# Kernel tuning notes

Hardware: AMD Instinct MI355X
Metric: run time of the kernel (lower is better)

## Reference

```python
import jax, jax.numpy as jnp
import numpy as np

N_NODES = 20000
N_EDGES = 200000
MUL = 16          # multiplicity of 0e and 1o in irreps_in/out
NUM_BASIS = 8
HIDDEN = 64
W_NUMEL = 4 * MUL * MUL  # 1024: four 'uvw' paths of 16x1x16 weights
INV_SQRT3 = 1.0 / np.sqrt(3.0)
PW0 = np.sqrt(1.0 / 32.0)  # path weight into 0e: sqrt(dim(0e)/(16+16))
PW1 = np.sqrt(3.0 / 32.0)  # path weight into 1o: sqrt(dim(1o)/(16+16))
SI_NORM = 1.0 / np.sqrt(MUL)  # o3.Linear fan-in normalization


def setup_inputs() -> dict:
    key = jax.random.key(0)
    ks = jax.random.split(key, 12)
    node_feat = jax.random.normal(ks[0], (N_NODES, 4 * MUL), dtype=jnp.float32)
    edge_attr = jax.random.uniform(ks[1], (N_EDGES, NUM_BASIS), dtype=jnp.float32)
    sh = jax.random.normal(ks[2], (N_EDGES, 4), dtype=jnp.float32)
    edge_index = jax.random.randint(ks[3], (2, N_EDGES), 0, N_NODES, dtype=jnp.int32)
    # radial MLP params (torch nn.Linear: y = x @ W.T + b; we store W already transposed)
    w1 = jax.random.normal(ks[4], (NUM_BASIS, HIDDEN), dtype=jnp.float32) * 0.3
    b1 = jax.random.normal(ks[5], (HIDDEN,), dtype=jnp.float32) * 0.1
    w2 = jax.random.normal(ks[6], (HIDDEN, W_NUMEL), dtype=jnp.float32) * 0.1
    b2 = jax.random.normal(ks[7], (W_NUMEL,), dtype=jnp.float32) * 0.1
    # o3.Linear self-interaction: one (mul_in, mul_out) block per irrep
    wsi0 = jax.random.normal(ks[8], (MUL, MUL), dtype=jnp.float32)
    wsi1 = jax.random.normal(ks[9], (MUL, MUL), dtype=jnp.float32)
    return {"node_feat": node_feat, "edge_attr": edge_attr, "sh": sh,
            "w1": w1, "b1": b1, "w2": w2, "b2": b2,
            "wsi0": wsi0, "wsi1": wsi1, "edge_index": edge_index}


def reference(node_feat, edge_attr, sh, w1, b1, w2, b2, wsi0, wsi1, edge_index):
    n_nodes = node_feat.shape[0]
    row, col = edge_index[0], edge_index[1]

    # per-edge tensor-product weights from radial basis
    h = jax.nn.silu(edge_attr @ w1 + b1)
    w = h @ w2 + b2                                   # [E, 1024]
    Wp = w.reshape(-1, 4, MUL, MUL)                    # 4 paths, each (u, w)

    # gathered source-node features, split into 0e scalars and 1o vectors
    xs = node_feat[col, :MUL]                          # [E, 16]
    xv = node_feat[col, MUL:].reshape(-1, MUL, 3)      # [E, 16, 3]
    y0 = sh[:, 0]                                      # [E]   0e part of sh
    y1 = sh[:, 1:4]                                    # [E,3] 1o part of sh

    # CG paths (e3nn FullyConnectedTensorProduct, component/element norm):
    # path0: 0e x 0e -> 0e (cg=1); path3: 1o x 1o -> 0e (cg=delta/sqrt3)
    dot = jnp.einsum('eum,em->eu', xv, y1)             # [E,16]
    out0 = PW0 * (jnp.einsum('euw,eu->ew', Wp[:, 0], xs * y0[:, None])
                  + INV_SQRT3 * jnp.einsum('euw,eu->ew', Wp[:, 3], dot))
    # path1: 0e x 1o -> 1o; path2: 1o x 0e -> 1o (cg=delta/sqrt3)
    outv = (PW1 * INV_SQRT3) * (
        jnp.einsum('euw,eu->ew', Wp[:, 1], xs)[:, :, None] * y1[:, None, :]
        + jnp.einsum('euw,eum->ewm', Wp[:, 2], xv) * y0[:, None, None])

    messages = jnp.concatenate([out0, outv.reshape(-1, 3 * MUL)], axis=-1)  # [E,64]
    agg = jax.ops.segment_sum(messages, row, num_segments=n_nodes)          # [N,64]

    # self-interaction: o3.Linear (block-diagonal per irrep, / sqrt(fan_in))
    si0 = (node_feat[:, :MUL] @ wsi0) * SI_NORM
    siv = jnp.einsum('num,uw->nwm', node_feat[:, MUL:].reshape(-1, MUL, 3), wsi1) * SI_NORM
    si = jnp.concatenate([si0, siv.reshape(-1, 3 * MUL)], axis=-1)
    return agg + si
```

## Files before the change

kernel.cpp:

```cpp
#include <hip/hip_runtime.h>
#include <hip/hip_bf16.h>

#define N_NODES_C 20000
#define N_EDGES_C 200000

#define PW0_C       0.17677669529663687f
#define PW1_C       0.30618621784789724f
#define INV_SQRT3_C 0.57735026918962576f
#define SI_NORM_C   0.25f

typedef __attribute__((ext_vector_type(8))) short short8;
typedef __attribute__((ext_vector_type(4))) float f32x4;

__device__ __forceinline__ unsigned short f2bf(float x) {
    union { float f; unsigned u; } v; v.f = x;
    unsigned r = v.u + 0x7fffu + ((v.u >> 16) & 1u);
    return (unsigned short)(r >> 16);
}

__global__ __launch_bounds__(256) void k_h(const float* __restrict__ ea,
                                           const float* __restrict__ w1,
                                           const float* __restrict__ b1,
                                           unsigned short* __restrict__ h) {
    int idx = blockIdx.x * 256 + threadIdx.x;
    int e = idx >> 6, c = idx & 63;
    const float* a = ea + e * 8;
    float acc = b1[c];
    #pragma unroll
    for (int k = 0; k < 8; ++k) acc = fmaf(a[k], w1[k * 64 + c], acc);
    float s = acc / (1.0f + __expf(-acc));
    h[idx] = f2bf(s);
}

__global__ __launch_bounds__(256) void k_w2(const float* __restrict__ w2,
                                            unsigned short* __restrict__ w2f) {
    int tid = blockIdx.x * 256 + threadIdx.x;
    int j  = tid & 7;
    int l  = (tid >> 3) & 63;
    int ks = (tid >> 9) & 1;
    int tp = tid >> 10;
    int u = tp >> 2, k = tp & 3;
    int krow = ks * 32 + (l >> 4) * 8 + j;
    int col  = k * 256 + u * 16 + (l & 15);
    w2f[tid] = f2bf(w2[krow * 1024 + col]);
}

__global__ __launch_bounds__(256) void k_si(const float* __restrict__ nf,
                                            const float* __restrict__ wsi0,
                                            const float* __restrict__ wsi1,
                                            float* __restrict__ out) {
    int idx = blockIdx.x * 256 + threadIdx.x;
    int n = idx >> 6, c = idx & 63;
    const float* x = nf + n * 64;
    float acc = 0.f;
    if (c < 16) {
        #pragma unroll
        for (int u = 0; u < 16; ++u) acc = fmaf(x[u], wsi0[u * 16 + c], acc);
    } else {
        int w = (c - 16) / 3, m = (c - 16) - w * 3;
        #pragma unroll
        for (int u = 0; u < 16; ++u) acc = fmaf(x[16 + u * 3 + m], wsi1[u * 16 + w], acc);
    }
    out[idx] = acc * SI_NORM_C;
}

__global__ __launch_bounds__(256) void k_main(const float* __restrict__ nf,
                                              const float* __restrict__ sh,
                                              const int* __restrict__ ei,
                                              const unsigned short* __restrict__ h,
                                              const unsigned short* __restrict__ w2f,
                                              const float* __restrict__ b2,
                                              float* __restrict__ out) {
    __shared__ unsigned short w2s[2][4096];
    __shared__ float S[6][16][64];
    __shared__ float sh_s[64][4];
    __shared__ float b2_s[4][16][16];
    __shared__ int   row_s[64];

    float (*nf_s)[64] = (float (*)[64])w2s;

    const int t    = threadIdx.x;
    const int e0   = blockIdx.x * 64;
    const int lane = t & 63;
    const int wid  = t >> 6;

    {
        float* b2flat = &b2_s[0][0][0];
        #pragma unroll
        for (int i = 0; i < 4; ++i) b2flat[t + i * 256] = b2[t + i * 256];
        int el = t >> 2, part = t & 3;
        int col = ei[N_EDGES_C + e0 + el];
        const f32x4* src = (const f32x4*)(nf + col * 64);
        #pragma unroll
        for (int q = 0; q < 4; ++q)
            *(f32x4*)&nf_s[el][part * 16 + q * 4] = src[part * 4 + q];
        if (part == 0) {
            *(f32x4*)&sh_s[el][0] = *(const f32x4*)(sh + (e0 + el) * 4);
            row_s[el] = ei[e0 + el];
        }
    }
    const unsigned short* hrow = h + (e0 + wid * 16 + (lane & 15)) * 64 + ((lane >> 4) * 8);
    short8 a0 = *(const short8*)(hrow);
    short8 a1 = *(const short8*)(hrow + 32);
    __syncthreads();

    int4 p0, p1;
    {
        const int4* wsrc = (const int4*)(w2f);
        p0 = wsrc[t]; p1 = wsrc[256 + t];
    }
    {
        int el = t >> 2, part = t & 3;
        float y0 = sh_s[el][0], y1x = sh_s[el][1], y1y = sh_s[el][2], y1z = sh_s[el][3];
        #pragma unroll
        for (int uu = 0; uu < 4; ++uu) {
            int u = part * 4 + uu;
            float xs = nf_s[el][u];
            float v0 = nf_s[el][16 + u * 3 + 0];
            float v1 = nf_s[el][16 + u * 3 + 1];
            float v2 = nf_s[el][16 + u * 3 + 2];
            float dot = v0 * y1x + v1 * y1y + v2 * y1z;
            S[0][u][el] = xs * y0;
            S[1][u][el] = xs;
            S[2][u][el] = v0;
            S[3][u][el] = v1;
            S[4][u][el] = v2;
            S[5][u][el] = INV_SQRT3_C * dot;
        }
    }
    __syncthreads();
    ((int4*)w2s[0])[t] = p0;
    ((int4*)w2s[0])[256 + t] = p1;
    __syncthreads();

    const int wcol = lane & 15;
    const int eS   = wid * 16 + ((lane >> 4) << 2);

    f32x4 acc0 = {0.f, 0.f, 0.f, 0.f};
    f32x4 tv1  = {0.f, 0.f, 0.f, 0.f};
    f32x4 t2a  = {0.f, 0.f, 0.f, 0.f};
    f32x4 t2b  = {0.f, 0.f, 0.f, 0.f};
    f32x4 t2c  = {0.f, 0.f, 0.f, 0.f};

    for (int u = 0; u < 16; ++u) {
        const int buf = u & 1;
        int4 n0, n1;
        if (u < 15) {
            const int4* wsrc = (const int4*)(w2f + (u + 1) * 4096);
            n0 = wsrc[t]; n1 = wsrc[256 + t];
        }
        f32x4 sA  = *(const f32x4*)&S[0][u][eS];
        f32x4 sX  = *(const f32x4*)&S[1][u][eS];
        f32x4 sV0 = *(const f32x4*)&S[2][u][eS];
        f32x4 sV1 = *(const f32x4*)&S[3][u][eS];
        f32x4 sV2 = *(const f32x4*)&S[4][u][eS];
        f32x4 sB  = *(const f32x4*)&S[5][u][eS];
        #pragma unroll
        for (int k = 0; k < 4; ++k) {
            short8 b0 = *(const short8*)&w2s[buf][(k * 2 + 0) * 512 + lane * 8];
            short8 b1 = *(const short8*)&w2s[buf][(k * 2 + 1) * 512 + lane * 8];
            f32x4 c = {0.f, 0.f, 0.f, 0.f};
            c = __builtin_amdgcn_mfma_f32_16x16x32_bf16(a0, b0, c, 0, 0, 0);
            c = __builtin_amdgcn_mfma_f32_16x16x32_bf16(a1, b1, c, 0, 0, 0);
            float bb = b2_s[k][u][wcol];
            if (k == 0) {
                #pragma unroll
                for (int r = 0; r < 4; ++r) acc0[r] = fmaf(c[r] + bb, sA[r], acc0[r]);
            } else if (k == 1) {
                #pragma unroll
                for (int r = 0; r < 4; ++r) tv1[r] = fmaf(c[r] + bb, sX[r], tv1[r]);
            } else if (k == 2) {
                #pragma unroll
                for (int r = 0; r < 4; ++r) {
                    float wp = c[r] + bb;
                    t2a[r] = fmaf(wp, sV0[r], t2a[r]);
                    t2b[r] = fmaf(wp, sV1[r], t2b[r]);
                    t2c[r] = fmaf(wp, sV2[r], t2c[r]);
                }
            } else {
                #pragma unroll
                for (int r = 0; r < 4; ++r) acc0[r] = fmaf(c[r] + bb, sB[r], acc0[r]);
            }
        }
        if (u < 15) {
            int4* dst = (int4*)w2s[buf ^ 1];
            dst[t] = n0; dst[256 + t] = n1;
        }
        __syncthreads();
    }

    #pragma unroll
    for (int r = 0; r < 4; ++r) {
        int el = eS + r;
        int node = row_s[el];
        float y0 = sh_s[el][0];
        float* dst = out + node * 64;
        atomicAdd(dst + wcol, PW0_C * acc0[r]);
        float tt1 = tv1[r];
        const float c1 = PW1_C * INV_SQRT3_C;
        atomicAdd(dst + 16 + wcol * 3 + 0, c1 * (tt1 * sh_s[el][1] + t2a[r] * y0));
        atomicAdd(dst + 16 + wcol * 3 + 1, c1 * (tt1 * sh_s[el][2] + t2b[r] * y0));
        atomicAdd(dst + 16 + wcol * 3 + 2, c1 * (tt1 * sh_s[el][3] + t2c[r] * y0));
    }
}

extern "C" void kernel_launch(void* const* d_in, const int* in_sizes, int n_in,
                              void* d_out, int out_size, void* d_ws, size_t ws_size,
                              hipStream_t stream) {
    const float* nf   = (const float*)d_in[0];
    const float* ea   = (const float*)d_in[1];
    const float* sh   = (const float*)d_in[2];
    const float* w1   = (const float*)d_in[3];
    const float* b1   = (const float*)d_in[4];
    const float* w2   = (const float*)d_in[5];
    const float* b2   = (const float*)d_in[6];
    const float* wsi0 = (const float*)d_in[7];
    const float* wsi1 = (const float*)d_in[8];
    const int*   ei   = (const int*)d_in[9];
    float* out = (float*)d_out;

    unsigned short* h   = (unsigned short*)d_ws;
    unsigned short* w2f = h + (size_t)N_EDGES_C * 64;

    k_h  <<<50000, 256, 0, stream>>>(ea, w1, b1, h);
    k_w2 <<<256,   256, 0, stream>>>(w2, w2f);
    k_si <<<5000,  256, 0, stream>>>(nf, wsi0, wsi1, out);
    k_main<<<3125, 256, 0, stream>>>(nf, sh, ei, h, w2f, b2, out);
}
```

Measured before the change: 175.7 us.

## Replace atomic scatter with CSR sort and per-node gather of edge messages

Instead of atomically adding each edge message into the output, the main kernel now writes per-edge messages to a workspace buffer. Count, scan and fill kernels build a CSR index of edges grouped by destination node, and a gather kernel sums each node's messages without atomics. The self-interaction linear is folded into that gather kernel. This removes float atomic contention but adds a 51 MB message write and re-read, a single-block serial scan, and more launches.

```diff
diff --git a/kernel.cpp b/kernel.cpp
--- a/kernel.cpp
+++ b/kernel.cpp
@@ -45,23 +45,50 @@
     w2f[tid] = f2bf(w2[krow * 1024 + col]);
 }
 
-__global__ __launch_bounds__(256) void k_si(const float* __restrict__ nf,
-                                            const float* __restrict__ wsi0,
-                                            const float* __restrict__ wsi1,
-                                            float* __restrict__ out) {
-    int idx = blockIdx.x * 256 + threadIdx.x;
-    int n = idx >> 6, c = idx & 63;
-    const float* x = nf + n * 64;
-    float acc = 0.f;
-    if (c < 16) {
-        #pragma unroll
-        for (int u = 0; u < 16; ++u) acc = fmaf(x[u], wsi0[u * 16 + c], acc);
-    } else {
-        int w = (c - 16) / 3, m = (c - 16) - w * 3;
-        #pragma unroll
-        for (int u = 0; u < 16; ++u) acc = fmaf(x[16 + u * 3 + m], wsi1[u * 16 + w], acc);
-    }
-    out[idx] = acc * SI_NORM_C;
+__global__ __launch_bounds__(256) void k_count(const int* __restrict__ ei,
+                                               int* __restrict__ cnt) {
+    int e = blockIdx.x * 256 + threadIdx.x;
+    if (e < N_EDGES_C) atomicAdd(&cnt[ei[e]], 1);
+}
+
+__global__ __launch_bounds__(256) void k_scan(const int* __restrict__ cnt,
+                                              int* __restrict__ base) {
+    __shared__ int wsum[4];
+    __shared__ int carry_s;
+    if (threadIdx.x == 0) carry_s = 0;
+    int lane = threadIdx.x & 63, wid = threadIdx.x >> 6;
+    for (int start = 0; start < N_NODES_C; start += 256) {
+        int i = start + threadIdx.x;
+        int v = (i < N_NODES_C) ? cnt[i] : 0;
+        int x = v;
+        #pragma unroll
+        for (int d = 1; d < 64; d <<= 1) {
+            int y = __shfl_up(x, d);
+            if (lane >= d) x += y;
+        }
+        if (lane == 63) wsum[wid] = x;
+        __syncthreads();
+        int woff = 0;
+        #pragma unroll
+        for (int w = 0; w < 4; ++w) if (w < wid) woff += wsum[w];
+        int carry = carry_s;
+        if (i < N_NODES_C) base[i] = carry + woff + x - v;
+        __syncthreads();
+        if (threadIdx.x == 255) carry_s = carry + woff + x;
+    }
+    if (threadIdx.x == 0) base[N_NODES_C] = N_EDGES_C;
+}
+
+__global__ __launch_bounds__(256) void k_fill(const int* __restrict__ ei,
+                                              const int* __restrict__ base,
+                                              int* __restrict__ cur,
+                                              int* __restrict__ eix) {
+    int e = blockIdx.x * 256 + threadIdx.x;
+    if (e < N_EDGES_C) {
+        int r = ei[e];
+        int p = atomicAdd(&cur[r], 1);
+        eix[base[r] + p] = e;
+    }
 }
 
 __global__ __launch_bounds__(256) void k_main(const float* __restrict__ nf,
@@ -70,12 +97,11 @@
                                               const unsigned short* __restrict__ h,
                                               const unsigned short* __restrict__ w2f,
                                               const float* __restrict__ b2,
-                                              float* __restrict__ out) {
+                                              float* __restrict__ msg) {
     __shared__ unsigned short w2s[2][4096];
     __shared__ float S[6][16][64];
     __shared__ float sh_s[64][4];
     __shared__ float b2_s[4][16][16];
-    __shared__ int   row_s[64];
 
     float (*nf_s)[64] = (float (*)[64])w2s;
 
@@ -94,10 +120,8 @@
         #pragma unroll
         for (int q = 0; q < 4; ++q)
             *(f32x4*)&nf_s[el][part * 16 + q * 4] = src[part * 4 + q];
-        if (part == 0) {
+        if (part == 0)
             *(f32x4*)&sh_s[el][0] = *(const f32x4*)(sh + (e0 + el) * 4);
-            row_s[el] = ei[e0 + el];
-        }
     }
     const unsigned short* hrow = h + (e0 + wid * 16 + (lane & 15)) * 64 + ((lane >> 4) * 8);
     short8 a0 = *(const short8*)(hrow);
@@ -192,16 +216,44 @@
     #pragma unroll
     for (int r = 0; r < 4; ++r) {
         int el = eS + r;
-        int node = row_s[el];
         float y0 = sh_s[el][0];
-        float* dst = out + node * 64;
-        atomicAdd(dst + wcol, PW0_C * acc0[r]);
+        float* dst = msg + (size_t)(e0 + el) * 64;
+        dst[wcol] = PW0_C * acc0[r];
         float tt1 = tv1[r];
         const float c1 = PW1_C * INV_SQRT3_C;
-        atomicAdd(dst + 16 + wcol * 3 + 0, c1 * (tt1 * sh_s[el][1] + t2a[r] * y0));
-        atomicAdd(dst + 16 + wcol * 3 + 1, c1 * (tt1 * sh_s[el][2] + t2b[r] * y0));
-        atomicAdd(dst + 16 + wcol * 3 + 2, c1 * (tt1 * sh_s[el][3] + t2c[r] * y0));
-    }
+        dst[16 + wcol * 3 + 0] = c1 * (tt1 * sh_s[el][1] + t2a[r] * y0);
+        dst[16 + wcol * 3 + 1] = c1 * (tt1 * sh_s[el][2] + t2b[r] * y0);
+        dst[16 + wcol * 3 + 2] = c1 * (tt1 * sh_s[el][3] + t2c[r] * y0);
+    }
+}
+
+__global__ __launch_bounds__(256) void k_gather(const float* __restrict__ msg,
+                                                const int* __restrict__ eix,
+                                                const int* __restrict__ base,
+                                                const float* __restrict__ nf,
+                                                const float* __restrict__ wsi0,
+                                                const float* __restrict__ wsi1,
+                                                float* __restrict__ out) {
+    int wid = threadIdx.x >> 6, lane = threadIdx.x & 63;
+    int n = blockIdx.x * 4 + wid;
+    if (n >= N_NODES_C) return;
+    int b0 = base[n], b1 = base[n + 1];
+    float acc = 0.f;
+    for (int j = b0; j < b1; ++j) {
+        int e = eix[j];
+        acc += msg[(size_t)e * 64 + lane];
+    }
+    const float* x = nf + n * 64;
+    float si = 0.f;
+    if (lane < 16) {
+        #pragma unroll
+        for (int u = 0; u < 16; ++u) si = fmaf(x[u], wsi0[u * 16 + lane], si);
+    } else {
+        int w = (lane - 16) / 3, m = (lane - 16) - w * 3;
+        #pragma unroll
+        for (int u = 0; u < 16; ++u) si = fmaf(x[16 + u * 3 + m], wsi1[u * 16 + w], si);
+    }
+    out[n * 64 + lane] = acc + si * SI_NORM_C;
 }
 
 extern "C" void kernel_launch(void* const* d_in, const int* in_sizes, int n_in,
@@ -219,11 +271,22 @@
     const int*   ei   = (const int*)d_in[9];
     float* out = (float*)d_out;
 
-    unsigned short* h   = (unsigned short*)d_ws;
-    unsigned short* w2f = h + (size_t)N_EDGES_C * 64;
-
-    k_h  <<<50000, 256, 0, stream>>>(ea, w1, b1, h);
-    k_w2 <<<256,   256, 0, stream>>>(w2, w2f);
-    k_si <<<5000,  256, 0, stream>>>(nf, wsi0, wsi1, out);
-    k_main<<<3125, 256, 0, stream>>>(nf, sh, ei, h, w2f, b2, out);
-}
+    char* ws = (char*)d_ws;
+    float* msg           = (float*)ws;
+    unsigned short* h    = (unsigned short*)(ws + 51200000);
+    unsigned short* w2f  = (unsigned short*)(ws + 51200000 + 25600000);
+    int* cnt             = (int*)(ws + 51200000 + 25600000 + 131072);
+    int* cur             = cnt + N_NODES_C;
+    int* base            = cur + N_NODES_C;
+    int* eix             = base + N_NODES_C + 1;
+
+    hipMemsetAsync(cnt, 0, 2 * N_NODES_C * sizeof(int), stream);
+
+    k_h    <<<50000, 256, 0, stream>>>(ea, w1, b1, h);
+    k_w2   <<<256,   256, 0, stream>>>(w2, w2f);
+    k_count<<<(N_EDGES_C + 255) / 256, 256, 0, stream>>>(ei, cnt);
+    k_scan <<<1,     256, 0, stream>>>(cnt, base);
+    k_fill <<<(N_EDGES_C + 255) / 256, 256, 0, stream>>>(ei, base, cur, eix);
+    k_main <<<3125,  256, 0, stream>>>(nf, sh, ei, h, w2f, b2, msg);
+    k_gather<<<5000, 256, 0, stream>>>(msg, eix, base, nf, wsi0, wsi1, out);
+}
```

After: 245.7 us. 1.4x slower.
